# Optimization experiments

Hardware: AMD Instinct MI355X
Metric: run time of the kernel (lower is better)

## Reference

```python
import jax, jax.numpy as jnp
import numpy as np

S, B, E, H = 2048, 2, 1024, 16
DH = E // H
SCALING = DH ** -0.5


def setup_inputs() -> dict:
    key = jax.random.key(0)
    ks = jax.random.split(key, 9)
    std = 1.0 / np.sqrt(E)
    return {
        "query": jax.random.normal(ks[0], (S, B, E), jnp.float32),
        "wq": jax.random.normal(ks[1], (E, E), jnp.float32) * std,
        "bq": jax.random.normal(ks[2], (E,), jnp.float32) * 0.02,
        "wk": jax.random.normal(ks[3], (E, E), jnp.float32) * std,
        "bk": jax.random.normal(ks[4], (E,), jnp.float32) * 0.02,
        "wv": jax.random.normal(ks[5], (E, E), jnp.float32) * std,
        "bv": jax.random.normal(ks[6], (E,), jnp.float32) * 0.02,
        "wo": jax.random.normal(ks[7], (E, E), jnp.float32) * std,
        "bo": jax.random.normal(ks[8], (E,), jnp.float32) * 0.02,
    }


def reference(query, wq, bq, wk, bk, wv, bv, wo, bo):
    # query: [S, B, E] (time, batch, channel), self-attention: key=value=query
    q = (query @ wq.T + bq) * SCALING          # fairseq scales q, not scores
    k = query @ wk.T + bk
    v = query @ wv.T + bv
    # split heads: [S, B, H, DH]
    q = q.reshape(S, B, H, DH)
    k = k.reshape(S, B, H, DH)
    v = v.reshape(S, B, H, DH)
    scores = jnp.einsum("qbhd,kbhd->bhqk", q, k)   # [B, H, S, S]
    probs = jax.nn.softmax(scores, axis=-1)
    ctx = jnp.einsum("bhqk,kbhd->qbhd", probs, v)  # [S, B, H, DH]
    ctx = ctx.reshape(S, B, E)
    return ctx @ wo.T + bo                          # [S, B, E]
```

## Files before the change

### kernel.cpp

```cpp
#include <hip/hip_runtime.h>
#include <hip/hip_bf16.h>
#include <stdint.h>

#define S_LEN 2048
#define BATCH 2
#define EMB   1024
#define NH    16
#define DHEAD 64
#define ROWS  (S_LEN*BATCH)
#define SCALE_Q 0.18033688011112042f
#define DEFER_THR 11.0f

typedef __attribute__((ext_vector_type(8))) short bf16x8;
typedef __attribute__((ext_vector_type(4))) float f32x4;

typedef const __attribute__((address_space(1))) void* gas_ptr;
typedef __attribute__((address_space(3))) void* las_ptr;
#define GLD16(g, l) __builtin_amdgcn_global_load_lds((gas_ptr)(g), (las_ptr)(l), 16, 0, 0)

__device__ __forceinline__ unsigned short f2b(float f) {
  union { float f; unsigned int u; } v; v.f = f;
  unsigned int u = v.u;
  unsigned int r = (u + 0x7FFFu + ((u >> 16) & 1u)) >> 16;
  return (unsigned short)r;
}

__device__ __forceinline__ unsigned cvt_pk_bf16(float lo, float hi) {
  unsigned r;
  asm("v_cvt_pk_bf16_f32 %0, %1, %2" : "=v"(r) : "v"(lo), "v"(hi));
  return r;
}

__device__ __forceinline__ void cvt8(const float* __restrict__ s,
                                     unsigned short* __restrict__ d, size_t i) {
  float4 a = *reinterpret_cast<const float4*>(s + i);
  float4 b = *reinterpret_cast<const float4*>(s + i + 4);
  uint4 o;
  o.x = (unsigned)f2b(a.x) | ((unsigned)f2b(a.y) << 16);
  o.y = (unsigned)f2b(a.z) | ((unsigned)f2b(a.w) << 16);
  o.z = (unsigned)f2b(b.x) | ((unsigned)f2b(b.y) << 16);
  o.w = (unsigned)f2b(b.z) | ((unsigned)f2b(b.w) << 16);
  *reinterpret_cast<uint4*>(d + i) = o;
}

__global__ __launch_bounds__(256) void cvt_kernel(const float* __restrict__ s,
                                                  unsigned short* __restrict__ d) {
  size_t i = ((size_t)blockIdx.x * 256 + threadIdx.x) * 8;
  cvt8(s, d, i);
}

__global__ __launch_bounds__(256) void cvt4_kernel(
    const float* __restrict__ s0, const float* __restrict__ s1,
    const float* __restrict__ s2, const float* __restrict__ s3,
    unsigned short* __restrict__ d0, unsigned short* __restrict__ d1,
    unsigned short* __restrict__ d2, unsigned short* __restrict__ d3) {
  const float* s; unsigned short* d;
  switch (blockIdx.y) {
    case 0:  s = s0; d = d0; break;
    case 1:  s = s1; d = d1; break;
    case 2:  s = s2; d = d2; break;
    default: s = s3; d = d3; break;
  }
  size_t i = ((size_t)blockIdx.x * 256 + threadIdx.x) * 8;
  cvt8(s, d, i);
}

__device__ __forceinline__ void gemm_mainloop(const unsigned short* __restrict__ A,
                                              const unsigned short* __restrict__ Bw,
                                              int m0, int n0, f32x4 acc[4][4]) {
  __shared__ unsigned short Ab[2][128 * 64];
  __shared__ unsigned short Bb[2][128 * 64];
  const int t    = threadIdx.x;
  const int lane = t & 63;
  const int w    = t >> 6;
  const int wr   = w >> 1, wc = w & 1;
  const int lm   = lane & 15;
  const int lq   = lane >> 4;

  f32x4 zf = {0.0f, 0.0f, 0.0f, 0.0f};
#pragma unroll
  for (int i = 0; i < 4; ++i)
#pragma unroll
    for (int j = 0; j < 4; ++j) acc[i][j] = zf;

  auto STAGE = [&](int b, int k0) {
#pragma unroll
    for (int q = 0; q < 4; ++q) {
      int c = t + q * 256;
      int r = c >> 3, ci = c & 7;
      int lc = ci ^ (r & 7);
      GLD16(A  + (size_t)(m0 + r) * EMB + k0 + lc * 8,
            (char*)&Ab[b][0] + (size_t)(q * 256 + w * 64) * 16);
      GLD16(Bw + (size_t)(n0 + r) * EMB + k0 + lc * 8,
            (char*)&Bb[b][0] + (size_t)(q * 256 + w * 64) * 16);
    }
  };

  STAGE(0, 0);
  asm volatile("s_waitcnt vmcnt(0)" ::: "memory");
  __syncthreads();

  int cur = 0;
  const int NT = EMB / 64;
  for (int it = 0; it < NT; ++it) {
    if (it + 1 < NT) STAGE(cur ^ 1, (it + 1) * 64);

#pragma unroll
    for (int kk = 0; kk < 2; ++kk) {
      bf16x8 af[4], bfr[4];
#pragma unroll
      for (int i = 0; i < 4; ++i) {
        int ra = wr * 64 + i * 16 + lm;
        af[i] = *reinterpret_cast<const bf16x8*>(
            &Ab[cur][ra * 64 + ((kk * 4 + lq) ^ (ra & 7)) * 8]);
      }
#pragma unroll
      for (int j = 0; j < 4; ++j) {
        int rb = wc * 64 + j * 16 + lm;
        bfr[j] = *reinterpret_cast<const bf16x8*>(
            &Bb[cur][rb * 64 + ((kk * 4 + lq) ^ (rb & 7)) * 8]);
      }
#pragma unroll
      for (int i = 0; i < 4; ++i)
#pragma unroll
        for (int j = 0; j < 4; ++j)
          acc[i][j] = __builtin_amdgcn_mfma_f32_16x16x32_bf16(af[i], bfr[j], acc[i][j], 0, 0, 0);
    }

    asm volatile("s_waitcnt vmcnt(0)" ::: "memory");
    __syncthreads();
    cur ^= 1;
  }
}

__global__ __launch_bounds__(256) void gemm_qkv_kernel(
    const unsigned short* __restrict__ X,
    const unsigned short* __restrict__ Wq, const unsigned short* __restrict__ Wk,
    const unsigned short* __restrict__ Wv,
    const float* __restrict__ bq, const float* __restrict__ bk, const float* __restrict__ bv,
    unsigned short* __restrict__ Qb, unsigned short* __restrict__ Kb,
    unsigned short* __restrict__ Vb) {
  const int m0 = blockIdx.x * 128;
  const int n0 = blockIdx.y * 128;
  const int z  = blockIdx.z;
  const unsigned short* Bw = (z == 0) ? Wq : (z == 1) ? Wk : Wv;
  const float* bias        = (z == 0) ? bq : (z == 1) ? bk : bv;
  unsigned short* Out      = (z == 0) ? Qb : (z == 1) ? Kb : Vb;
  const float scale        = (z == 0) ? SCALE_Q : 1.0f;

  f32x4 acc[4][4];
  gemm_mainloop(X, Bw, m0, n0, acc);

  const int lane = threadIdx.x & 63;
  const int w    = threadIdx.x >> 6;
  const int wr   = w >> 1, wc = w & 1;
  const int lm   = lane & 15, lq = lane >> 4;
#pragma unroll
  for (int j = 0; j < 4; ++j) {
    int col = n0 + wc * 64 + j * 16 + lm;
    int h = col >> 6, dd = col & 63;
    float bc = bias[col];
#pragma unroll
    for (int i = 0; i < 4; ++i) {
#pragma unroll
      for (int r = 0; r < 4; ++r) {
        int row = m0 + wr * 64 + i * 16 + lq * 4 + r;
        int s = row >> 1, b = row & 1;
        float v = (acc[i][j][r] + bc) * scale;
        Out[((size_t)(b * NH + h) * S_LEN + s) * DHEAD + dd] = f2b(v);
      }
    }
  }
}

__global__ __launch_bounds__(256) void gemm_out_kernel(
    const unsigned short* __restrict__ Ctx, const unsigned short* __restrict__ Wo,
    const float* __restrict__ bo, float* __restrict__ Out) {
  const int m0 = blockIdx.x * 128;
  const int n0 = blockIdx.y * 128;
  f32x4 acc[4][4];
  gemm_mainloop(Ctx, Wo, m0, n0, acc);

  const int lane = threadIdx.x & 63;
  const int w    = threadIdx.x >> 6;
  const int wr   = w >> 1, wc = w & 1;
  const int lm   = lane & 15, lq = lane >> 4;
#pragma unroll
  for (int j = 0; j < 4; ++j) {
    int col = n0 + wc * 64 + j * 16 + lm;
    float bc = bo[col];
#pragma unroll
    for (int i = 0; i < 4; ++i) {
#pragma unroll
      for (int r = 0; r < 4; ++r) {
        int row = m0 + wr * 64 + i * 16 + lq * 4 + r;
        Out[(size_t)row * EMB + col] = acc[i][j][r] + bc;
      }
    }
  }
}

__global__ __launch_bounds__(256) void transpose_v_kernel(
    const unsigned short* __restrict__ Vb, unsigned short* __restrict__ Vtg) {
  const int bh = blockIdx.x;
  const int kb = blockIdx.y * 64;
  const unsigned short* src = Vb + (size_t)bh * S_LEN * DHEAD;
  unsigned short* dst = Vtg + (size_t)bh * DHEAD * S_LEN;
  __shared__ unsigned short T[64][80];
  const int t = threadIdx.x;
#pragma unroll
  for (int q = 0; q < 2; ++q) {
    int c = t + q * 256;
    int r = c >> 3, j = (c & 7) * 8;
    bf16x8 v = *reinterpret_cast<const bf16x8*>(src + (size_t)(kb + r) * DHEAD + j);
    *reinterpret_cast<bf16x8*>(&T[r][j]) = v;
  }
  __syncthreads();
  int d = t >> 2, kvc = (t & 3) * 16;
  bf16x8 o0, o1;
#pragma unroll
  for (int e = 0; e < 8; ++e) o0[e] = (short)T[kvc + e][d];
#pragma unroll
  for (int e = 0; e < 8; ++e) o1[e] = (short)T[kvc + 8 + e][d];
  *reinterpret_cast<bf16x8*>(dst + (size_t)d * S_LEN + kb + kvc) = o0;
  *reinterpret_cast<bf16x8*>(dst + (size_t)d * S_LEN + kb + kvc + 8) = o1;
}

__global__ __launch_bounds__(512) void attn_kernel(
    const unsigned short* __restrict__ Qb, const unsigned short* __restrict__ Kb,
    const unsigned short* __restrict__ Vtg, unsigned short* __restrict__ Ctx) {
  const int bh = blockIdx.x;
  const int q0 = blockIdx.y * 128;
  const int t    = threadIdx.x;
  const int lane = t & 63;
  const int w    = t >> 6;
  const int lm   = lane & 15, lq = lane >> 4;
  const unsigned short* Q  = Qb  + (size_t)bh * S_LEN * DHEAD;
  const unsigned short* K  = Kb  + (size_t)bh * S_LEN * DHEAD;
  const unsigned short* Vt = Vtg + (size_t)bh * DHEAD * S_LEN;

  __shared__ unsigned short Kl[2][64 * 64];
  __shared__ unsigned short Vl[2][64 * 64];
  __shared__ unsigned short Pl[8][16 * 72];

  const int qw = q0 + w * 16;

  bf16x8 aq[2];
#pragma unroll
  for (int c = 0; c < 2; ++c)
    aq[c] = *reinterpret_cast<const bf16x8*>(
        Q + (size_t)(qw + lm) * DHEAD + c * 32 + lq * 8);

  f32x4 zf = {0.0f, 0.0f, 0.0f, 0.0f};
  f32x4 accO[4];
#pragma unroll
  for (int ni = 0; ni < 4; ++ni) accO[ni] = zf;
  float m_s = -1e30f, l_s = 0.0f;

  auto STAGE = [&](int b, int kb) {
    int r = t >> 3, p = t & 7;
    int lc = p ^ (r & 7);
    GLD16(K  + (size_t)(kb + r) * DHEAD + lc * 8,
          (char*)&Kl[b][0] + (size_t)(w * 64) * 16);
    GLD16(Vt + (size_t)r * S_LEN + kb + lc * 8,
          (char*)&Vl[b][0] + (size_t)(w * 64) * 16);
  };

  STAGE(0, 0);
  asm volatile("s_waitcnt vmcnt(0)" ::: "memory");
  __syncthreads();

  int cur = 0;
  const int NT = S_LEN / 64;
  for (int it = 0; it < NT; ++it) {
    if (it + 1 < NT) STAGE(cur ^ 1, (it + 1) * 64);

    f32x4 p4[4];
    __builtin_amdgcn_s_setprio(1);
#pragma unroll
    for (int ji = 0; ji < 4; ++ji) {
      int rr = ji * 16 + lm;
      bf16x8 k0 = *reinterpret_cast<const bf16x8*>(
          &Kl[cur][rr * 64 + ((lq) ^ (rr & 7)) * 8]);
      bf16x8 k1 = *reinterpret_cast<const bf16x8*>(
          &Kl[cur][rr * 64 + ((4 + lq) ^ (rr & 7)) * 8]);
      f32x4 s0 = __builtin_amdgcn_mfma_f32_16x16x32_bf16(k0, aq[0], zf, 0, 0, 0);
      p4[ji]   = __builtin_amdgcn_mfma_f32_16x16x32_bf16(k1, aq[1], s0, 0, 0, 0);
    }
    __builtin_amdgcn_s_setprio(0);

    float t0 = fmaxf(fmaxf(p4[0][0], p4[0][1]), fmaxf(p4[0][2], p4[0][3]));
    float t1 = fmaxf(fmaxf(p4[1][0], p4[1][1]), fmaxf(p4[1][2], p4[1][3]));
    float t2 = fmaxf(fmaxf(p4[2][0], p4[2][1]), fmaxf(p4[2][2], p4[2][3]));
    float t3 = fmaxf(fmaxf(p4[3][0], p4[3][1]), fmaxf(p4[3][2], p4[3][3]));
    float tm = fmaxf(fmaxf(t0, t1), fmaxf(t2, t3));
    tm = fmaxf(tm, __shfl_xor(tm, 16));
    tm = fmaxf(tm, __shfl_xor(tm, 32));

    if (!__all(tm - m_s <= DEFER_THR)) {
      float mn = fmaxf(m_s, tm);
      float sc = exp2f(m_s - mn);
      l_s *= sc;
      m_s = mn;
#pragma unroll
      for (int r = 0; r < 4; ++r) {
        float scr = __shfl(sc, lq * 4 + r);
#pragma unroll
        for (int ni = 0; ni < 4; ++ni) accO[ni][r] *= scr;
      }
    }

    float ps = 0.0f;
#pragma unroll
    for (int ji = 0; ji < 4; ++ji)
#pragma unroll
      for (int r = 0; r < 4; ++r) {
        float e = exp2f(p4[ji][r] - m_s);
        p4[ji][r] = e;
        ps += e;
      }
    ps += __shfl_xor(ps, 16);
    ps += __shfl_xor(ps, 32);
    l_s += ps;

    unsigned short* Pw = &Pl[w][0];
#pragma unroll
    for (int ji = 0; ji < 4; ++ji) {
      uint2 u;
      u.x = cvt_pk_bf16(p4[ji][0], p4[ji][1]);
      u.y = cvt_pk_bf16(p4[ji][2], p4[ji][3]);
      *reinterpret_cast<uint2*>(&Pw[lm * 72 + ji * 16 + lq * 4]) = u;
    }

    bf16x8 ap[2];
#pragma unroll
    for (int c = 0; c < 2; ++c)
      ap[c] = *reinterpret_cast<const bf16x8*>(&Pw[lm * 72 + c * 32 + lq * 8]);
    __builtin_amdgcn_s_setprio(1);
#pragma unroll
    for (int ni = 0; ni < 4; ++ni) {
      int dd = ni * 16 + lm;
#pragma unroll
      for (int c = 0; c < 2; ++c) {
        bf16x8 bv = *reinterpret_cast<const bf16x8*>(
            &Vl[cur][dd * 64 + ((c * 4 + lq) ^ (dd & 7)) * 8]);
        accO[ni] = __builtin_amdgcn_mfma_f32_16x16x32_bf16(ap[c], bv, accO[ni], 0, 0, 0);
      }
    }
    __builtin_amdgcn_s_setprio(0);

    asm volatile("s_waitcnt vmcnt(0)" ::: "memory");
    __syncthreads();
    cur ^= 1;
  }

  const int b = bh >> 4, h = bh & 15;
#pragma unroll
  for (int r = 0; r < 4; ++r) {
    float rl = 1.0f / __shfl(l_s, lq * 4 + r);
    int srow = qw + lq * 4 + r;
    size_t rowbase = ((size_t)srow * BATCH + b) * EMB + (size_t)h * 64;
#pragma unroll
    for (int ni = 0; ni < 4; ++ni)
      Ctx[rowbase + ni * 16 + lm] = f2b(accO[ni][r] * rl);
  }
}

extern "C" void kernel_launch(void* const* d_in, const int* in_sizes, int n_in,
                              void* d_out, int out_size, void* d_ws, size_t ws_size,
                              hipStream_t stream) {
  const float* query = (const float*)d_in[0];
  const float* wq = (const float*)d_in[1];
  const float* bq = (const float*)d_in[2];
  const float* wk = (const float*)d_in[3];
  const float* bk = (const float*)d_in[4];
  const float* wv = (const float*)d_in[5];
  const float* bv = (const float*)d_in[6];
  const float* wo = (const float*)d_in[7];
  const float* bo = (const float*)d_in[8];
  float* out = (float*)d_out;

  unsigned short* p = (unsigned short*)d_ws;
  unsigned short* Xbf = p;                        p += (size_t)ROWS * EMB;
  unsigned short* Wqb = p;                        p += (size_t)EMB * EMB;
  unsigned short* Wkb = p;                        p += (size_t)EMB * EMB;
  unsigned short* Wvb = p;                        p += (size_t)EMB * EMB;
  unsigned short* Wob = p;                        p += (size_t)EMB * EMB;
  unsigned short* Qb  = p;                        p += (size_t)ROWS * EMB;
  unsigned short* Kb  = p;                        p += (size_t)ROWS * EMB;
  unsigned short* Vb  = p;                        p += (size_t)ROWS * EMB;
  unsigned short* Ctx = p;                        p += (size_t)ROWS * EMB;
  unsigned short* Vtg = Xbf;

  cvt_kernel<<<ROWS * EMB / 8 / 256, 256, 0, stream>>>(query, Xbf);
  cvt4_kernel<<<dim3(EMB * EMB / 8 / 256, 4), 256, 0, stream>>>(
      wq, wk, wv, wo, Wqb, Wkb, Wvb, Wob);
  gemm_qkv_kernel<<<dim3(ROWS / 128, EMB / 128, 3), 256, 0, stream>>>(
      Xbf, Wqb, Wkb, Wvb, bq, bk, bv, Qb, Kb, Vb);
  transpose_v_kernel<<<dim3(BATCH * NH, S_LEN / 64), 256, 0, stream>>>(Vb, Vtg);
  attn_kernel<<<dim3(BATCH * NH, S_LEN / 128), 512, 0, stream>>>(Qb, Kb, Vtg, Ctx);
  gemm_out_kernel<<<dim3(ROWS / 128, EMB / 128), 256, 0, stream>>>(Ctx, Wob, bo, out);
}
```

Measured before the change: 222.6 us.

## Single-buffer GEMM mainloop and deepen attention K/V prefetch with vmcnt-based waits

```diff
diff --git a/kernel.cpp b/kernel.cpp
--- a/kernel.cpp
+++ b/kernel.cpp
@@ -68,8 +68,8 @@
 __device__ __forceinline__ void gemm_mainloop(const unsigned short* __restrict__ A,
                                               const unsigned short* __restrict__ Bw,
                                               int m0, int n0, f32x4 acc[4][4]) {
-  __shared__ unsigned short Ab[2][128 * 64];
-  __shared__ unsigned short Bb[2][128 * 64];
+  __shared__ unsigned short Ab[128 * 64];
+  __shared__ unsigned short Bb[128 * 64];
   const int t    = threadIdx.x;
   const int lane = t & 63;
   const int w    = t >> 6;
@@ -83,27 +83,19 @@
 #pragma unroll
     for (int j = 0; j < 4; ++j) acc[i][j] = zf;
 
-  auto STAGE = [&](int b, int k0) {
+  for (int k0 = 0; k0 < EMB; k0 += 64) {
 #pragma unroll
     for (int q = 0; q < 4; ++q) {
       int c = t + q * 256;
       int r = c >> 3, ci = c & 7;
       int lc = ci ^ (r & 7);
       GLD16(A  + (size_t)(m0 + r) * EMB + k0 + lc * 8,
-            (char*)&Ab[b][0] + (size_t)(q * 256 + w * 64) * 16);
+            (char*)&Ab[0] + (size_t)(q * 256 + w * 64) * 16);
       GLD16(Bw + (size_t)(n0 + r) * EMB + k0 + lc * 8,
-            (char*)&Bb[b][0] + (size_t)(q * 256 + w * 64) * 16);
-    }
-  };
-
-  STAGE(0, 0);
-  asm volatile("s_waitcnt vmcnt(0)" ::: "memory");
-  __syncthreads();
-
-  int cur = 0;
-  const int NT = EMB / 64;
-  for (int it = 0; it < NT; ++it) {
-    if (it + 1 < NT) STAGE(cur ^ 1, (it + 1) * 64);
+            (char*)&Bb[0] + (size_t)(q * 256 + w * 64) * 16);
+    }
+    asm volatile("s_waitcnt vmcnt(0)" ::: "memory");
+    __syncthreads();
 
 #pragma unroll
     for (int kk = 0; kk < 2; ++kk) {
@@ -112,13 +104,13 @@
       for (int i = 0; i < 4; ++i) {
         int ra = wr * 64 + i * 16 + lm;
         af[i] = *reinterpret_cast<const bf16x8*>(
-            &Ab[cur][ra * 64 + ((kk * 4 + lq) ^ (ra & 7)) * 8]);
+            &Ab[ra * 64 + ((kk * 4 + lq) ^ (ra & 7)) * 8]);
       }
 #pragma unroll
       for (int j = 0; j < 4; ++j) {
         int rb = wc * 64 + j * 16 + lm;
         bfr[j] = *reinterpret_cast<const bf16x8*>(
-            &Bb[cur][rb * 64 + ((kk * 4 + lq) ^ (rb & 7)) * 8]);
+            &Bb[rb * 64 + ((kk * 4 + lq) ^ (rb & 7)) * 8]);
       }
 #pragma unroll
       for (int i = 0; i < 4; ++i)
@@ -126,10 +118,7 @@
         for (int j = 0; j < 4; ++j)
           acc[i][j] = __builtin_amdgcn_mfma_f32_16x16x32_bf16(af[i], bfr[j], acc[i][j], 0, 0, 0);
     }
-
-    asm volatile("s_waitcnt vmcnt(0)" ::: "memory");
     __syncthreads();
-    cur ^= 1;
   }
 }
 
@@ -266,14 +255,18 @@
           (char*)&Vl[b][0] + (size_t)(w * 64) * 16);
   };
 
+  const int NT = S_LEN / 64;
   STAGE(0, 0);
-  asm volatile("s_waitcnt vmcnt(0)" ::: "memory");
-  __syncthreads();
-
-  int cur = 0;
-  const int NT = S_LEN / 64;
+  STAGE(1, 64);
+
   for (int it = 0; it < NT; ++it) {
-    if (it + 1 < NT) STAGE(cur ^ 1, (it + 1) * 64);
+    const int cur = it & 1;
+    if (it < NT - 1) {
+      asm volatile("s_waitcnt vmcnt(2)" ::: "memory");
+    } else {
+      asm volatile("s_waitcnt vmcnt(0)" ::: "memory");
+    }
+    __builtin_amdgcn_s_barrier();
 
     f32x4 p4[4];
     __builtin_amdgcn_s_setprio(1);
@@ -349,9 +342,11 @@
     }
     __builtin_amdgcn_s_setprio(0);
 
-    asm volatile("s_waitcnt vmcnt(0)" ::: "memory");
-    __syncthreads();
-    cur ^= 1;
+    asm volatile("s_waitcnt lgkmcnt(0)" ::: "memory");
+    __builtin_amdgcn_sched_barrier(0);
+    __builtin_amdgcn_s_barrier();
+
+    if (it + 2 < NT) STAGE(cur, (it + 2) * 64);
   }
 
   const int b = bh >> 4, h = bh & 15;
```

Measured after the change: 222.4 us. No clear change (-0.1%).
